# Kernel tuning notes

Measured on AMD Instinct MI355X. Metric: run time of the kernel, lower is better.

Reference implementation:

```python
import jax, jax.numpy as jnp
import numpy as np

B, N, D, C = 64, 512, 1024, 4  # batch, num_electrodes, d_model, num_classes
H = D // 2


def setup_inputs() -> dict:
    key = jax.random.key(0)
    ks = jax.random.split(key, 16)
    s = 0.02
    return {
        "Q": jax.random.normal(ks[0], (B, N, D), jnp.float32),
        "K": jax.random.normal(ks[1], (B, N, D), jnp.float32),
        "V": jax.random.normal(ks[2], (B, N, D), jnp.float32),
        "electrode_ids": jnp.arange(N, dtype=jnp.int64 if jax.config.jax_enable_x64 else jnp.int32),
        "emb": jax.random.normal(ks[3], (N, D), jnp.float32) * s,
        "dw1": jax.random.normal(ks[4], (H, D), jnp.float32) * s,
        "db1": jnp.zeros((H,), jnp.float32),
        "dw2": jax.random.normal(ks[5], (1, H), jnp.float32) * s,
        "db2": jnp.zeros((1,), jnp.float32),
        "sw1": jax.random.normal(ks[6], (H, D), jnp.float32) * s,
        "sb1": jnp.zeros((H,), jnp.float32),
        "sw2": jax.random.normal(ks[7], (1, H), jnp.float32) * s,
        "sb2": jnp.zeros((1,), jnp.float32),
        "dopamine_scale": jnp.asarray(1.0, jnp.float32),
        "serotonin_scale": jnp.asarray(1.0, jnp.float32),
        "fc_w": jax.random.normal(ks[8], (C, N * D), jnp.float32) * s,
        "fc_b": jnp.zeros((C,), jnp.float32),
    }


def reference(Q, K, V, electrode_ids, emb, dw1, db1, dw2, db2,
              sw1, sb1, sw2, sb2, dopamine_scale, serotonin_scale, fc_w, fc_b):
    e = emb[electrode_ids]                       # [N, D]
    Q = Q + e
    K = K + e
    V = V + e
    scale = jnp.sqrt(jnp.asarray(D, jnp.float32))
    scores = jnp.einsum('bnd,bmd->bnm', Q, K) / scale          # [B, N, N]
    probs = jax.nn.softmax(scores, axis=-1)
    entropy = -jnp.sum(probs * jnp.log(probs + 1e-6), axis=-1)  # [B, N]

    # dopamine MLP on Q tokens (eval mode -> dropout is identity)
    dh = jax.nn.relu(jnp.einsum('bnd,hd->bnh', Q, dw1) + db1)
    dopamine = jax.nn.sigmoid(jnp.einsum('bnh,oh->bno', dh, dw2) + db2)[..., 0]  # [B, N]

    # serotonin MLP on entropy broadcast to D identical features:
    # Linear(entropy * ones(D)) == entropy * W1.sum(axis=1) + b1 (same math, no [B,N,D] temp)
    sh = jax.nn.relu(entropy[..., None] * jnp.sum(sw1, axis=1) + sb1)            # [B, N, H]
    serotonin = jax.nn.sigmoid(jnp.einsum('bnh,oh->bno', sh, sw2) + sb2)[..., 0]  # [B, N]

    mod = dopamine_scale * dopamine[..., None] - serotonin_scale * serotonin[..., None]
    ms = scores + mod
    mu = jnp.mean(ms, axis=-1, keepdims=True)
    sd = jnp.std(ms, axis=-1, keepdims=True, ddof=1)  # torch.std default is unbiased
    ms = (ms - mu) / (sd + 1e-6)
    probs2 = jax.nn.softmax(ms, axis=-1)
    attn_out = jnp.einsum('bnm,bmd->bnd', probs2, V)   # [B, N, D]
    flat = attn_out.reshape(attn_out.shape[0], -1)      # [B, N*D]
    return flat @ fc_w.T + fc_b                          # [B, C]
```

## Files before the change

### kernel.cpp

```cpp
#include <hip/hip_runtime.h>

#define NN 512
#define ND 1024
#define NDW 524288
#define NBATCH 64

typedef __attribute__((ext_vector_type(8))) __bf16 bf16x8;
typedef __attribute__((ext_vector_type(4))) float f32x4;
typedef unsigned short u16;
typedef unsigned int u32;

__device__ __forceinline__ u16 f2bf(float x) {
    u32 u = __float_as_uint(x);
    u = (u + 0x7fffu + ((u >> 16) & 1u)) >> 16;
    return (u16)u;
}

__global__ __launch_bounds__(256)
void prep_all(const float* __restrict__ Q, const float* __restrict__ K,
              const float* __restrict__ V, const int* __restrict__ eid,
              const float* __restrict__ emb,
              u16* __restrict__ Qe, u16* __restrict__ Ke, u16* __restrict__ VT,
              float* __restrict__ out, const float* __restrict__ fcb)
{
    __shared__ u16 T[64 * 72];
    const int bb = blockIdx.x;
    const int tid = threadIdx.x;

    if (bb < 16384) {
        size_t f = ((size_t)bb * 256 + tid) * 8;
        int n = (int)((f >> 10) & (NN - 1));
        int col = (int)(f & (ND - 1));
        const float* ep = emb + (size_t)eid[n] * ND + col;
        float4 e0 = *(const float4*)ep, e1 = *(const float4*)(ep + 4);
        {
            const float* qp = Q + f;
            float4 x0 = *(const float4*)qp, x1 = *(const float4*)(qp + 4);
            union { uint4 u; u16 s[8]; } o;
            o.s[0]=f2bf(x0.x+e0.x); o.s[1]=f2bf(x0.y+e0.y); o.s[2]=f2bf(x0.z+e0.z); o.s[3]=f2bf(x0.w+e0.w);
            o.s[4]=f2bf(x1.x+e1.x); o.s[5]=f2bf(x1.y+e1.y); o.s[6]=f2bf(x1.z+e1.z); o.s[7]=f2bf(x1.w+e1.w);
            *(uint4*)(Qe + f) = o.u;
        }
        {
            const float* kp = K + f;
            float4 x0 = *(const float4*)kp, x1 = *(const float4*)(kp + 4);
            union { uint4 u; u16 s[8]; } o;
            o.s[0]=f2bf(x0.x+e0.x); o.s[1]=f2bf(x0.y+e0.y); o.s[2]=f2bf(x0.z+e0.z); o.s[3]=f2bf(x0.w+e0.w);
            o.s[4]=f2bf(x1.x+e1.x); o.s[5]=f2bf(x1.y+e1.y); o.s[6]=f2bf(x1.z+e1.z); o.s[7]=f2bf(x1.w+e1.w);
            *(uint4*)(Ke + f) = o.u;
        }
    } else if (bb < 16384 + 8192) {
        const int t = bb - 16384;
        const int n0 = (t & 7) * 64, d0 = ((t >> 3) & 15) * 64, b = t >> 7;
        {
            const int r = tid >> 2, cs = (tid & 3) * 16;
            const int n = n0 + r;
            const float* vp = V + ((size_t)b * NN + n) * ND + d0 + cs;
            const float* ep = emb + (size_t)eid[n] * ND + d0 + cs;
            #pragma unroll
            for (int j = 0; j < 4; ++j) {
                float4 v = *(const float4*)(vp + j * 4);
                float4 e = *(const float4*)(ep + j * 4);
                T[(cs + j*4 + 0) * 72 + r] = f2bf(v.x + e.x);
                T[(cs + j*4 + 1) * 72 + r] = f2bf(v.y + e.y);
                T[(cs + j*4 + 2) * 72 + r] = f2bf(v.z + e.z);
                T[(cs + j*4 + 3) * 72 + r] = f2bf(v.w + e.w);
            }
        }
        __syncthreads();
        {
            const int dr = tid >> 2, ms = (tid & 3) * 16;
            u16* dst = VT + ((size_t)b * ND + d0 + dr) * NN + n0 + ms;
            *(uint4*)dst       = *(const uint4*)&T[dr * 72 + ms];
            *(uint4*)(dst + 8) = *(const uint4*)&T[dr * 72 + ms + 8];
        }
    } else {
        if (tid < NBATCH * 4) out[tid] = fcb[tid & 3];
    }
}

__global__ __launch_bounds__(256)
void nma_attn(const u16* __restrict__ Qe, const u16* __restrict__ Ke,
              const u16* __restrict__ VT, const float* __restrict__ fcw,
              float* __restrict__ out)
{
    __shared__ __align__(16) u16 Ps[32 * 520];
    __shared__ float red[4][32][4];
    __shared__ float rowM[32], rowInv[32], rowRden[32];

    const int tid  = threadIdx.x;
    const int w    = tid >> 6;
    const int lane = tid & 63;
    const int q    = lane >> 4;
    const int l15  = lane & 15;
    const int bid  = blockIdx.x;
    const int jj   = bid >> 3;
    const int b    = (bid & 7) + ((jj >> 4) << 3);
    const int i0   = (jj & 15) * 32;
    const size_t bOff = (size_t)b * NN * ND;
    const int wrow = w * 128;

    f32x4 acc[2][8];
    #pragma unroll
    for (int it = 0; it < 2; ++it)
        #pragma unroll
        for (int mt = 0; mt < 8; ++mt)
            acc[it][mt] = (f32x4){0.f, 0.f, 0.f, 0.f};

    {
        const u16* aP0 = Qe + bOff + (size_t)(i0 + l15) * ND + q * 8;
        const u16* aP1 = aP0 + (size_t)16 * ND;
        const u16* bP  = Ke + bOff + (size_t)(wrow + l15) * ND + q * 8;
        for (int kc = 0; kc < 32; ++kc) {
            const int ko = kc * 32;
            bf16x8 a0 = *(const bf16x8*)(aP0 + ko);
            bf16x8 a1 = *(const bf16x8*)(aP1 + ko);
            #pragma unroll
            for (int mt = 0; mt < 8; ++mt) {
                bf16x8 bf = *(const bf16x8*)(bP + (size_t)(mt * 16) * ND + ko);
                acc[0][mt] = __builtin_amdgcn_mfma_f32_16x16x32_bf16(a0, bf, acc[0][mt], 0, 0, 0);
                acc[1][mt] = __builtin_amdgcn_mfma_f32_16x16x32_bf16(a1, bf, acc[1][mt], 0, 0, 0);
            }
        }
    }

    const float SC = 0.03125f;
    #pragma unroll
    for (int it = 0; it < 2; ++it)
        #pragma unroll
        for (int mt = 0; mt < 8; ++mt) {
            acc[it][mt][0] *= SC; acc[it][mt][1] *= SC;
            acc[it][mt][2] *= SC; acc[it][mt][3] *= SC;
        }
    float ssum[2][4], ssq[2][4], smax[2][4];
    #pragma unroll
    for (int it = 0; it < 2; ++it)
        #pragma unroll
        for (int r = 0; r < 4; ++r) {
            float s = 0.f, s2 = 0.f, mx = -3.4e38f;
            #pragma unroll
            for (int mt = 0; mt < 8; ++mt) {
                float v = acc[it][mt][r];
                s += v; s2 += v * v; mx = fmaxf(mx, v);
            }
            #pragma unroll
            for (int d = 1; d < 16; d <<= 1) {
                s  += __shfl_xor(s, d);
                s2 += __shfl_xor(s2, d);
                mx  = fmaxf(mx, __shfl_xor(mx, d));
            }
            ssum[it][r] = s; ssq[it][r] = s2; smax[it][r] = mx;
        }
    if (l15 == 0) {
        #pragma unroll
        for (int it = 0; it < 2; ++it)
            #pragma unroll
            for (int r = 0; r < 4; ++r) {
                int i = it * 16 + q * 4 + r;
                red[w][i][0] = ssum[it][r];
                red[w][i][1] = ssq[it][r];
                red[w][i][2] = smax[it][r];
            }
    }
    __syncthreads();
    if (tid < 32) {
        float s  = red[0][tid][0] + red[1][tid][0] + red[2][tid][0] + red[3][tid][0];
        float s2 = red[0][tid][1] + red[1][tid][1] + red[2][tid][1] + red[3][tid][1];
        float mx = fmaxf(fmaxf(red[0][tid][2], red[1][tid][2]),
                         fmaxf(red[2][tid][2], red[3][tid][2]));
        float mu  = s * (1.f / 512.f);
        float var = fmaxf((s2 - s * mu) * (1.f / 511.f), 0.f);
        float sd  = sqrtf(var);
        rowM[tid]   = mx;
        rowInv[tid] = 1.f / (sd + 1e-6f);
    }
    __syncthreads();
    float dsum[2][4];
    #pragma unroll
    for (int it = 0; it < 2; ++it)
        #pragma unroll
        for (int r = 0; r < 4; ++r) {
            int i = it * 16 + q * 4 + r;
            float M = rowM[i], inv = rowInv[i];
            float s = 0.f;
            #pragma unroll
            for (int mt = 0; mt < 8; ++mt) {
                float e = __expf((acc[it][mt][r] - M) * inv);
                acc[it][mt][r] = e; s += e;
            }
            #pragma unroll
            for (int d = 1; d < 16; d <<= 1) s += __shfl_xor(s, d);
            dsum[it][r] = s;
        }
    if (l15 == 0) {
        #pragma unroll
        for (int it = 0; it < 2; ++it)
            #pragma unroll
            for (int r = 0; r < 4; ++r)
                red[w][it * 16 + q * 4 + r][0] = dsum[it][r];
    }
    __syncthreads();
    if (tid < 32)
        rowRden[tid] = 1.f / (red[0][tid][0] + red[1][tid][0] + red[2][tid][0] + red[3][tid][0]);
    __syncthreads();
    #pragma unroll
    for (int it = 0; it < 2; ++it)
        #pragma unroll
        for (int r = 0; r < 4; ++r) {
            int i = it * 16 + q * 4 + r;
            float rd = rowRden[i];
            #pragma unroll
            for (int mt = 0; mt < 8; ++mt) {
                int m = w * 128 + mt * 16 + l15;
                Ps[i * 520 + m] = f2bf(acc[it][mt][r] * rd);
            }
        }
    __syncthreads();

    float fsum[4] = {0.f, 0.f, 0.f, 0.f};
    for (int h = 0; h < 2; ++h) {
        f32x4 oacc[2][8];
        #pragma unroll
        for (int it = 0; it < 2; ++it)
            #pragma unroll
            for (int dt = 0; dt < 8; ++dt)
                oacc[it][dt] = (f32x4){0.f, 0.f, 0.f, 0.f};
        const u16* vP = VT + (size_t)b * ND * NN
                      + (size_t)(h * 512 + wrow + l15) * NN + q * 8;
        for (int mc = 0; mc < 16; ++mc) {
            bf16x8 p0 = *(const bf16x8*)&Ps[l15 * 520 + mc * 32 + q * 8];
            bf16x8 p1 = *(const bf16x8*)&Ps[(16 + l15) * 520 + mc * 32 + q * 8];
            #pragma unroll
            for (int dt = 0; dt < 8; ++dt) {
                bf16x8 bf = *(const bf16x8*)(vP + (size_t)(dt * 16) * NN + mc * 32);
                oacc[0][dt] = __builtin_amdgcn_mfma_f32_16x16x32_bf16(p0, bf, oacc[0][dt], 0, 0, 0);
                oacc[1][dt] = __builtin_amdgcn_mfma_f32_16x16x32_bf16(p1, bf, oacc[1][dt], 0, 0, 0);
            }
        }
        #pragma unroll
        for (int it = 0; it < 2; ++it) {
            #pragma unroll
            for (int r = 0; r < 4; ++r) {
                const int iglob = i0 + it * 16 + q * 4 + r;
                const float* fr = fcw + (size_t)iglob * ND + (h * 512 + wrow + l15);
                #pragma unroll
                for (int dt = 0; dt < 8; ++dt) {
                    const float o = oacc[it][dt][r];
                    fsum[0] += o * fr[dt * 16];
                    fsum[1] += o * fr[(size_t)NDW + dt * 16];
                    fsum[2] += o * fr[(size_t)2 * NDW + dt * 16];
                    fsum[3] += o * fr[(size_t)3 * NDW + dt * 16];
                }
            }
        }
    }
    #pragma unroll
    for (int c = 0; c < 4; ++c)
        #pragma unroll
        for (int d = 1; d < 64; d <<= 1)
            fsum[c] += __shfl_xor(fsum[c], d);
    if (lane == 0) {
        red[w][0][0] = fsum[0]; red[w][0][1] = fsum[1];
        red[w][0][2] = fsum[2]; red[w][0][3] = fsum[3];
    }
    __syncthreads();
    if (tid < 4) {
        float s = red[0][0][tid] + red[1][0][tid] + red[2][0][tid] + red[3][0][tid];
        atomicAdd(&out[b * 4 + tid], s);
    }
}

extern "C" void kernel_launch(void* const* d_in, const int* in_sizes, int n_in,
                              void* d_out, int out_size, void* d_ws, size_t ws_size,
                              hipStream_t stream) {
    (void)in_sizes; (void)n_in; (void)ws_size; (void)out_size;
    const float* Q   = (const float*)d_in[0];
    const float* K   = (const float*)d_in[1];
    const float* V   = (const float*)d_in[2];
    const int*   eid = (const int*)d_in[3];
    const float* emb = (const float*)d_in[4];
    const float* fcw = (const float*)d_in[15];
    const float* fcb = (const float*)d_in[16];
    float* out = (float*)d_out;

    u16* Qe = (u16*)d_ws;
    u16* Ke = Qe + (size_t)NBATCH * NN * ND;
    u16* VT = Ke + (size_t)NBATCH * NN * ND;

    prep_all<<<dim3(16384 + 8192 + 1), dim3(256), 0, stream>>>(
        Q, K, V, eid, emb, Qe, Ke, VT, out, fcb);
    nma_attn<<<dim3(1024), dim3(256), 0, stream>>>(Qe, Ke, VT, fcw, out);
}
```

Before: 790.3 us.

## Fuse Q embedding into attention and stage K/V tiles via async LDS loads

Drops the separate bf16 Q buffer: the attention kernel now reads fp32 Q and the embedding directly, adds and converts them in registers, and prefetches the next chunk while the current one is computed. K and V^T tiles are brought into shared memory with global_load_lds DMA, double-buffered against the MFMA work through explicit waitcnt. This removes a full write and read of Qe. In exchange it adds 32KB of LDS, which may lower occupancy. Each wave reloads fp32 Q (twice the bytes of bf16) from every block that uses it.

```diff
diff --git a/kernel.cpp b/kernel.cpp
--- a/kernel.cpp
+++ b/kernel.cpp
@@ -16,11 +16,19 @@
     return (u16)u;
 }
 
+union BF8 { bf16x8 v; u16 s[8]; };
+
+__device__ __forceinline__ void dma16(const u16* g, const u16* l) {
+    __builtin_amdgcn_global_load_lds(
+        (const __attribute__((address_space(1))) u32*)(uintptr_t)g,
+        (__attribute__((address_space(3))) u32*)(u32)(uintptr_t)l,
+        16, 0, 0);
+}
+
 __global__ __launch_bounds__(256)
-void prep_all(const float* __restrict__ Q, const float* __restrict__ K,
-              const float* __restrict__ V, const int* __restrict__ eid,
-              const float* __restrict__ emb,
-              u16* __restrict__ Qe, u16* __restrict__ Ke, u16* __restrict__ VT,
+void prep_all(const float* __restrict__ K, const float* __restrict__ V,
+              const int* __restrict__ eid, const float* __restrict__ emb,
+              u16* __restrict__ Ke, u16* __restrict__ VT,
               float* __restrict__ out, const float* __restrict__ fcb)
 {
     __shared__ u16 T[64 * 72];
@@ -33,22 +41,12 @@
         int col = (int)(f & (ND - 1));
         const float* ep = emb + (size_t)eid[n] * ND + col;
         float4 e0 = *(const float4*)ep, e1 = *(const float4*)(ep + 4);
-        {
-            const float* qp = Q + f;
-            float4 x0 = *(const float4*)qp, x1 = *(const float4*)(qp + 4);
-            union { uint4 u; u16 s[8]; } o;
-            o.s[0]=f2bf(x0.x+e0.x); o.s[1]=f2bf(x0.y+e0.y); o.s[2]=f2bf(x0.z+e0.z); o.s[3]=f2bf(x0.w+e0.w);
-            o.s[4]=f2bf(x1.x+e1.x); o.s[5]=f2bf(x1.y+e1.y); o.s[6]=f2bf(x1.z+e1.z); o.s[7]=f2bf(x1.w+e1.w);
-            *(uint4*)(Qe + f) = o.u;
-        }
-        {
-            const float* kp = K + f;
-            float4 x0 = *(const float4*)kp, x1 = *(const float4*)(kp + 4);
-            union { uint4 u; u16 s[8]; } o;
-            o.s[0]=f2bf(x0.x+e0.x); o.s[1]=f2bf(x0.y+e0.y); o.s[2]=f2bf(x0.z+e0.z); o.s[3]=f2bf(x0.w+e0.w);
-            o.s[4]=f2bf(x1.x+e1.x); o.s[5]=f2bf(x1.y+e1.y); o.s[6]=f2bf(x1.z+e1.z); o.s[7]=f2bf(x1.w+e1.w);
-            *(uint4*)(Ke + f) = o.u;
-        }
+        const float* kp = K + f;
+        float4 x0 = *(const float4*)kp, x1 = *(const float4*)(kp + 4);
+        union { uint4 u; u16 s[8]; } o;
+        o.s[0]=f2bf(x0.x+e0.x); o.s[1]=f2bf(x0.y+e0.y); o.s[2]=f2bf(x0.z+e0.z); o.s[3]=f2bf(x0.w+e0.w);
+        o.s[4]=f2bf(x1.x+e1.x); o.s[5]=f2bf(x1.y+e1.y); o.s[6]=f2bf(x1.z+e1.z); o.s[7]=f2bf(x1.w+e1.w);
+        *(uint4*)(Ke + f) = o.u;
     } else if (bb < 16384 + 8192) {
         const int t = bb - 16384;
         const int n0 = (t & 7) * 64, d0 = ((t >> 3) & 15) * 64, b = t >> 7;
@@ -80,10 +78,12 @@
 }
 
 __global__ __launch_bounds__(256)
-void nma_attn(const u16* __restrict__ Qe, const u16* __restrict__ Ke,
+void nma_attn(const float* __restrict__ Q, const int* __restrict__ eid,
+              const float* __restrict__ emb, const u16* __restrict__ Ke,
               const u16* __restrict__ VT, const float* __restrict__ fcw,
               float* __restrict__ out)
 {
+    __shared__ __align__(16) u16 KV[NN * 32];
     __shared__ __align__(16) u16 Ps[32 * 520];
     __shared__ float red[4][32][4];
     __shared__ float rowM[32], rowInv[32], rowRden[32];
@@ -93,6 +93,8 @@
     const int lane = tid & 63;
     const int q    = lane >> 4;
     const int l15  = lane & 15;
+    const int rr   = lane >> 2;
+    const int seg  = lane & 3;
     const int bid  = blockIdx.x;
     const int jj   = bid >> 3;
     const int b    = (bid & 7) + ((jj >> 4) << 3);
@@ -100,6 +102,40 @@
     const size_t bOff = (size_t)b * NN * ND;
     const int wrow = w * 128;
 
+    const float* Qr0 = Q + bOff + (size_t)(i0 + l15) * ND;
+    const float* Qr1 = Q + bOff + (size_t)(i0 + 16 + l15) * ND;
+    const float* Er0 = emb + (size_t)eid[i0 + l15] * ND;
+    const float* Er1 = emb + (size_t)eid[i0 + 16 + l15] * ND;
+
+    const u16* KeB = Ke + bOff;
+    const u16* VTB = VT + (size_t)b * ND * NN;
+
+#define DMA_KE(KC) do {                                                         \
+    _Pragma("unroll")                                                           \
+    for (int ii_ = 0; ii_ < 8; ++ii_)                                           \
+        dma16(KeB + (size_t)(wrow + ii_ * 16 + rr) * ND + (KC) * 32 + seg * 8,  \
+              &KV[(wrow + ii_ * 16) * 32]);                                     \
+    } while (0)
+
+#define DMA_VT(H, MC) do {                                                      \
+    _Pragma("unroll")                                                           \
+    for (int ii_ = 0; ii_ < 8; ++ii_)                                           \
+        dma16(VTB + (size_t)((H) * 512 + wrow + ii_ * 16 + rr) * NN             \
+                  + (MC) * 32 + seg * 8,                                        \
+              &KV[(wrow + ii_ * 16) * 32]);                                     \
+    } while (0)
+
+#define LOADQ(DST, KOFF) do {                                                   \
+    DST[0] = *(const float4*)(Qr0 + (KOFF));                                    \
+    DST[1] = *(const float4*)(Qr0 + (KOFF) + 4);                                \
+    DST[2] = *(const float4*)(Er0 + (KOFF));                                    \
+    DST[3] = *(const float4*)(Er0 + (KOFF) + 4);                                \
+    DST[4] = *(const float4*)(Qr1 + (KOFF));                                    \
+    DST[5] = *(const float4*)(Qr1 + (KOFF) + 4);                                \
+    DST[6] = *(const float4*)(Er1 + (KOFF));                                    \
+    DST[7] = *(const float4*)(Er1 + (KOFF) + 4);                                \
+    } while (0)
+
     f32x4 acc[2][8];
     #pragma unroll
     for (int it = 0; it < 2; ++it)
@@ -107,21 +143,41 @@
         for (int mt = 0; mt < 8; ++mt)
             acc[it][mt] = (f32x4){0.f, 0.f, 0.f, 0.f};
 
+    float4 cur[8], nxt[8];
     {
-        const u16* aP0 = Qe + bOff + (size_t)(i0 + l15) * ND + q * 8;
-        const u16* aP1 = aP0 + (size_t)16 * ND;
-        const u16* bP  = Ke + bOff + (size_t)(wrow + l15) * ND + q * 8;
-        for (int kc = 0; kc < 32; ++kc) {
-            const int ko = kc * 32;
-            bf16x8 a0 = *(const bf16x8*)(aP0 + ko);
-            bf16x8 a1 = *(const bf16x8*)(aP1 + ko);
-            #pragma unroll
-            for (int mt = 0; mt < 8; ++mt) {
-                bf16x8 bf = *(const bf16x8*)(bP + (size_t)(mt * 16) * ND + ko);
-                acc[0][mt] = __builtin_amdgcn_mfma_f32_16x16x32_bf16(a0, bf, acc[0][mt], 0, 0, 0);
-                acc[1][mt] = __builtin_amdgcn_mfma_f32_16x16x32_bf16(a1, bf, acc[1][mt], 0, 0, 0);
-            }
-        }
+        LOADQ(cur, q * 8);
+        DMA_KE(0);
+    }
+
+#define P2BODY(KC, CUR, NXT) do {                                               \
+    asm volatile("s_waitcnt vmcnt(0)" ::: "memory");    \
+    bf16x8 bfr[8];                                                              \
+    _Pragma("unroll")                                                           \
+    for (int mt = 0; mt < 8; ++mt)                                              \
+        bfr[mt] = *(const bf16x8*)&KV[(wrow + mt * 16 + l15) * 32 + q * 8];     \
+    BF8 a0u, a1u;                                                               \
+    a0u.s[0]=f2bf(CUR[0].x+CUR[2].x); a0u.s[1]=f2bf(CUR[0].y+CUR[2].y);         \
+    a0u.s[2]=f2bf(CUR[0].z+CUR[2].z); a0u.s[3]=f2bf(CUR[0].w+CUR[2].w);         \
+    a0u.s[4]=f2bf(CUR[1].x+CUR[3].x); a0u.s[5]=f2bf(CUR[1].y+CUR[3].y);         \
+    a0u.s[6]=f2bf(CUR[1].z+CUR[3].z); a0u.s[7]=f2bf(CUR[1].w+CUR[3].w);         \
+    a1u.s[0]=f2bf(CUR[4].x+CUR[6].x); a1u.s[1]=f2bf(CUR[4].y+CUR[6].y);         \
+    a1u.s[2]=f2bf(CUR[4].z+CUR[6].z); a1u.s[3]=f2bf(CUR[4].w+CUR[6].w);         \
+    a1u.s[4]=f2bf(CUR[5].x+CUR[7].x); a1u.s[5]=f2bf(CUR[5].y+CUR[7].y);         \
+    a1u.s[6]=f2bf(CUR[5].z+CUR[7].z); a1u.s[7]=f2bf(CUR[5].w+CUR[7].w);         \
+    asm volatile("s_waitcnt lgkmcnt(0)" ::: "memory");    \
+    if ((KC) < 31) {                                                            \
+        DMA_KE((KC) + 1);                    \
+        LOADQ(NXT, ((KC) + 1) * 32 + q * 8);       \
+    }                                                                           \
+    _Pragma("unroll")                                                           \
+    for (int mt = 0; mt < 8; ++mt) {                                            \
+        acc[0][mt] = __builtin_amdgcn_mfma_f32_16x16x32_bf16(a0u.v, bfr[mt], acc[0][mt], 0, 0, 0); \
+        acc[1][mt] = __builtin_amdgcn_mfma_f32_16x16x32_bf16(a1u.v, bfr[mt], acc[1][mt], 0, 0, 0); \
+    } } while (0)
+
+    for (int kc = 0; kc < 32; kc += 2) {
+        P2BODY(kc, cur, nxt);
+        P2BODY(kc + 1, nxt, cur);
     }
 
     const float SC = 0.03125f;
@@ -217,6 +273,7 @@
         }
     __syncthreads();
 
+    DMA_VT(0, 0);
     float fsum[4] = {0.f, 0.f, 0.f, 0.f};
     for (int h = 0; h < 2; ++h) {
         f32x4 oacc[2][8];
@@ -225,16 +282,24 @@
             #pragma unroll
             for (int dt = 0; dt < 8; ++dt)
                 oacc[it][dt] = (f32x4){0.f, 0.f, 0.f, 0.f};
-        const u16* vP = VT + (size_t)b * ND * NN
-                      + (size_t)(h * 512 + wrow + l15) * NN + q * 8;
         for (int mc = 0; mc < 16; ++mc) {
             bf16x8 p0 = *(const bf16x8*)&Ps[l15 * 520 + mc * 32 + q * 8];
             bf16x8 p1 = *(const bf16x8*)&Ps[(16 + l15) * 520 + mc * 32 + q * 8];
+            asm volatile("s_waitcnt vmcnt(0)" ::: "memory");
+            bf16x8 bfr[8];
+            #pragma unroll
+            for (int dt = 0; dt < 8; ++dt)
+                bfr[dt] = *(const bf16x8*)&KV[(wrow + dt * 16 + l15) * 32 + q * 8];
+            asm volatile("s_waitcnt lgkmcnt(0)" ::: "memory");
+            const int j = h * 16 + mc;
+            if (j < 31) {
+                const int jn = j + 1;
+                DMA_VT(jn >> 4, jn & 15);
+            }
             #pragma unroll
             for (int dt = 0; dt < 8; ++dt) {
-                bf16x8 bf = *(const bf16x8*)(vP + (size_t)(dt * 16) * NN + mc * 32);
-                oacc[0][dt] = __builtin_amdgcn_mfma_f32_16x16x32_bf16(p0, bf, oacc[0][dt], 0, 0, 0);
-                oacc[1][dt] = __builtin_amdgcn_mfma_f32_16x16x32_bf16(p1, bf, oacc[1][dt], 0, 0, 0);
+                oacc[0][dt] = __builtin_amdgcn_mfma_f32_16x16x32_bf16(p0, bfr[dt], oacc[0][dt], 0, 0, 0);
+                oacc[1][dt] = __builtin_amdgcn_mfma_f32_16x16x32_bf16(p1, bfr[dt], oacc[1][dt], 0, 0, 0);
             }
         }
         #pragma unroll
@@ -268,6 +333,10 @@
         float s = red[0][0][tid] + red[1][0][tid] + red[2][0][tid] + red[3][0][tid];
         atomicAdd(&out[b * 4 + tid], s);
     }
+#undef P2BODY
+#undef LOADQ
+#undef DMA_KE
+#undef DMA_VT
 }
 
 extern "C" void kernel_launch(void* const* d_in, const int* in_sizes, int n_in,
@@ -283,11 +352,10 @@
     const float* fcb = (const float*)d_in[16];
     float* out = (float*)d_out;
 
-    u16* Qe = (u16*)d_ws;
-    u16* Ke = Qe + (size_t)NBATCH * NN * ND;
+    u16* Ke = (u16*)d_ws;
     u16* VT = Ke + (size_t)NBATCH * NN * ND;
 
     prep_all<<<dim3(16384 + 8192 + 1), dim3(256), 0, stream>>>(
-        Q, K, V, eid, emb, Qe, Ke, VT, out, fcb);
-    nma_attn<<<dim3(1024), dim3(256), 0, stream>>>(Qe, Ke, VT, fcw, out);
-}
+        K, V, eid, emb, Ke, VT, out, fcb);
+    nma_attn<<<dim3(1024), dim3(256), 0, stream>>>(Q, eid, emb, Ke, VT, fcw, out);
+}
```

Measured after the change: 717.2 us. 9.3% less time.
